# Performance work log

Measured on AMD Instinct MI355X. Metric: run time of the kernel, lower is better.

The kernel has to match this reference:

```python
import jax, jax.numpy as jnp
import numpy as np

IN_F = 1024
OUT_F = 1024
B, S = 8, 4096


def _pack_ternary(tern):
    # encoding: -1 -> 0, 0 -> 1, +1 -> 2; 4 values per byte, matching torch pack_ternary_weights
    enc = (tern + 1.0).astype(jnp.int32).reshape(-1)  # length divisible by 4 here
    return (enc[0::4] | (enc[1::4] << 2) | (enc[2::4] << 4) | (enc[3::4] << 6)).astype(jnp.int32)


def setup_inputs() -> dict:
    key = jax.random.key(0)
    kx, kw = jax.random.split(key)
    x = jax.random.normal(kx, (B, S, IN_F), dtype=jnp.float32)
    w = jax.random.normal(kw, (OUT_F, IN_F), dtype=jnp.float32) * 0.02
    # quantize_weights_158bit
    scale = jnp.maximum(jnp.mean(jnp.abs(w)), 1e-5)
    wn = w / scale
    tern = jnp.sign(wn) * (jnp.abs(wn) > 0.5).astype(jnp.float32)
    packed = _pack_ternary(tern)
    bias = jnp.zeros((OUT_F,), dtype=jnp.float32)
    return {"x": x, "packed_weight": packed, "weight_scale": scale.reshape(1), "bias": bias}


def reference(x, packed_weight, weight_scale, bias):
    n = OUT_F * IN_F
    shifts = jnp.array([0, 2, 4, 6], dtype=jnp.int32)
    # Faithful to original unpack_ternary_weights: concatenate bit-planes, then truncate.
    # (This is a permutation of the packed order, replicated deliberately.)
    enc = ((packed_weight[None, :] >> shifts[:, None]) & 3).reshape(-1)[:n]
    w = (enc.astype(jnp.float32) - 1.0).reshape(OUT_F, IN_F) * weight_scale  # dequant ternary
    # training path: INT8 per-token activation fake-quant
    act_scale = 127.0 / jnp.maximum(jnp.max(jnp.abs(x), axis=-1, keepdims=True), 1e-5)
    x_dq = jnp.clip(jnp.round(x * act_scale), -128.0, 127.0) / act_scale
    return jnp.einsum('bsi,oi->bso', x_dq, w) + bias
```

## Files before the change

kernel.cpp:

```cpp
#include <hip/hip_runtime.h>
#include <hip/hip_bf16.h>
#include <stdint.h>

typedef int i32x4 __attribute__((ext_vector_type(4)));

constexpr int IN_F = 1024;
constexpr int OUT_F = 1024;
constexpr int M_TOT = 8 * 4096;
constexpr int K_TOT = 1024;
constexpr int N_TOT = 1024;

__global__ __launch_bounds__(256) void quant_kernel(
    const float* __restrict__ x,
    const float* __restrict__ wscale,
    const int* __restrict__ packed,
    int8_t* __restrict__ q,
    float* __restrict__ inv_row,
    int8_t* __restrict__ wt)
{
    const int row = blockIdx.x;
    const int t = threadIdx.x;
    const float4 v = reinterpret_cast<const float4*>(x + (size_t)row * IN_F)[t];
    float m = fmaxf(fmaxf(fabsf(v.x), fabsf(v.y)), fmaxf(fabsf(v.z), fabsf(v.w)));
    #pragma unroll
    for (int off = 32; off > 0; off >>= 1)
        m = fmaxf(m, __shfl_xor(m, off));
    __shared__ float smax[4];
    if ((t & 63) == 0) smax[t >> 6] = m;
    __syncthreads();
    m = fmaxf(fmaxf(smax[0], smax[1]), fmaxf(smax[2], smax[3]));
    const float a = fmaxf(m, 1e-5f);
    const float as = 127.0f / a;

    char4 o;
    o.x = (char)(int)fminf(fmaxf(rintf(v.x * as), -128.0f), 127.0f);
    o.y = (char)(int)fminf(fmaxf(rintf(v.y * as), -128.0f), 127.0f);
    o.z = (char)(int)fminf(fmaxf(rintf(v.z * as), -128.0f), 127.0f);
    o.w = (char)(int)fminf(fmaxf(rintf(v.w * as), -128.0f), 127.0f);
    reinterpret_cast<char4*>(q + (size_t)row * IN_F)[t] = o;
    if (t == 0) inv_row[row] = (a / 127.0f) * wscale[0];

    if (row < OUT_F) {
        const int oo = row;
        const int k0 = t * 4;
        const int sh = (oo >> 8) * 2;
        const int pbase = ((oo & 255) << 10) + k0;
        const int4 pw = *reinterpret_cast<const int4*>(packed + pbase);
        char4 r;
        r.x = (char)(((pw.x >> sh) & 3) - 1);
        r.y = (char)(((pw.y >> sh) & 3) - 1);
        r.z = (char)(((pw.z >> sh) & 3) - 1);
        r.w = (char)(((pw.w >> sh) & 3) - 1);
        *reinterpret_cast<char4*>(wt + (size_t)oo * IN_F + k0) = r;
    }
}

constexpr int BM = 256, BN = 256, BK = 128;
constexpr int NT = K_TOT / BK;

__global__ __launch_bounds__(512, 2) void gemm_kernel(
    const int8_t* __restrict__ qa,
    const int8_t* __restrict__ wb,
    const float* __restrict__ inv_row,
    const float* __restrict__ bias,
    float* __restrict__ out)
{
    int bid = blockIdx.x;
    bid = (bid & 7) * ((int)gridDim.x >> 3) + (bid >> 3);
    const int tm = bid >> 2;
    const int tn = bid & 3;

    const int tid = threadIdx.x;
    const int lane = tid & 63;
    const int wid = tid >> 6;
    const int wr = wid >> 2;
    const int wc = wid & 3;

    __shared__ int8_t lds[2][2][2][128 * 128];

    const int rowA0 = tm * BM;
    const int rowB0 = tn * BN;
    const int frow = lane & 15;
    const int fq = lane >> 4;

    i32x4 acc[8][4] = {};

    auto stage = [&](int buf, int ab, int region, int kt) {
        const int8_t* base = ab ? wb : qa;
        #pragma unroll
        for (int j = 0; j < 2; ++j) {
            const int c = j * 512 + tid;
            const int rl = c >> 3, cc = c & 7;
            const int grow = ab ? (rowB0 + region * 128 + rl)
                                : (rowA0 + (rl & 64) * 2 + region * 64 + (rl & 63));
            const int scc = cc ^ (rl & 7);
            const int8_t* src = base + (size_t)grow * K_TOT + kt * BK + scc * 16;
            __builtin_amdgcn_global_load_lds(
                (const __attribute__((address_space(1))) void*)src,
                (__attribute__((address_space(3))) void*)&lds[buf][ab][region][c * 16],
                16, 0, 0);
        }
    };

    auto ldA = [&](int buf, int region, int mf, int ks) -> i32x4 {
        const int local = wr * 64 + (mf & 3) * 16 + frow;
        const int ch = (ks * 4 + fq) ^ (local & 7);
        return *reinterpret_cast<const i32x4*>(&lds[buf][0][region][local * 128 + ch * 16]);
    };
    auto ldB = [&](int buf, int nf, int ks) -> i32x4 {
        const int region = wc >> 1;
        const int local = (wc & 1) * 64 + nf * 16 + frow;
        const int ch = (ks * 4 + fq) ^ (local & 7);
        return *reinterpret_cast<const i32x4*>(&lds[buf][1][region][local * 128 + ch * 16]);
    };

    i32x4 aF[4][2], bF[4][2], aG[4][2];

    stage(0, 1, 0, 0); stage(0, 1, 1, 0); stage(0, 0, 0, 0); stage(0, 0, 1, 0);
    asm volatile("s_waitcnt vmcnt(0)" ::: "memory");
    __builtin_amdgcn_s_barrier();
    #pragma unroll
    for (int mf = 0; mf < 4; ++mf)
        #pragma unroll
        for (int ks = 0; ks < 2; ++ks)
            aF[mf][ks] = ldA(0, 0, mf, ks);
    #pragma unroll
    for (int nf = 0; nf < 4; ++nf)
        #pragma unroll
        for (int ks = 0; ks < 2; ++ks)
            bF[nf][ks] = ldB(0, nf, ks);

    #pragma unroll 1
    for (int T = 0; T < NT; ++T) {
        const int cur = T & 1, nxt = cur ^ 1;
        const bool st = (T + 1 < NT);

        #pragma unroll
        for (int mf = 0; mf < 4; ++mf)
            #pragma unroll
            for (int ks = 0; ks < 2; ++ks)
                aG[mf][ks] = ldA(cur, 1, mf, ks);
        if (st) {
            stage(nxt, 1, 0, T + 1); stage(nxt, 1, 1, T + 1);
            stage(nxt, 0, 0, T + 1); stage(nxt, 0, 1, T + 1);
        }

        asm volatile("s_waitcnt lgkmcnt(8)" ::: "memory");
        __builtin_amdgcn_sched_barrier(0);
        __builtin_amdgcn_s_setprio(1);
        #pragma unroll
        for (int mf = 0; mf < 4; ++mf)
            #pragma unroll
            for (int nf = 0; nf < 4; ++nf)
                #pragma unroll
                for (int ks = 0; ks < 2; ++ks)
                    acc[mf][nf] = __builtin_amdgcn_mfma_i32_16x16x64_i8(
                        aF[mf][ks], bF[nf][ks], acc[mf][nf], 0, 0, 0);
        __builtin_amdgcn_s_setprio(0);

        asm volatile("s_waitcnt lgkmcnt(0)" ::: "memory");
        __builtin_amdgcn_sched_barrier(0);
        __builtin_amdgcn_s_setprio(1);
        #pragma unroll
        for (int mf = 0; mf < 4; ++mf)
            #pragma unroll
            for (int nf = 0; nf < 4; ++nf)
                #pragma unroll
                for (int ks = 0; ks < 2; ++ks)
                    acc[4 + mf][nf] = __builtin_amdgcn_mfma_i32_16x16x64_i8(
                        aG[mf][ks], bF[nf][ks], acc[4 + mf][nf], 0, 0, 0);
        __builtin_amdgcn_s_setprio(0);

        if (st) {
            asm volatile("s_waitcnt vmcnt(0)" ::: "memory");
            __builtin_amdgcn_s_barrier();
            #pragma unroll
            for (int mf = 0; mf < 4; ++mf)
                #pragma unroll
                for (int ks = 0; ks < 2; ++ks)
                    aF[mf][ks] = ldA(nxt, 0, mf, ks);
            #pragma unroll
            for (int nf = 0; nf < 4; ++nf)
                #pragma unroll
                for (int ks = 0; ks < 2; ++ks)
                    bF[nf][ks] = ldB(nxt, nf, ks);
        }
    }

    #pragma unroll
    for (int mi = 0; mi < 8; ++mi) {
        #pragma unroll
        for (int j = 0; j < 4; ++j) {
            const int gm = rowA0 + wr * 128 + mi * 16 + fq * 4 + j;
            const float sc = inv_row[gm];
            #pragma unroll
            for (int nf = 0; nf < 4; ++nf) {
                const int gn = rowB0 + wc * 64 + nf * 16 + frow;
                __builtin_nontemporal_store(
                    (float)acc[mi][nf][j] * sc + bias[gn],
                    &out[(size_t)gm * N_TOT + gn]);
            }
        }
    }
}

extern "C" void kernel_launch(void* const* d_in, const int* in_sizes, int n_in,
                              void* d_out, int out_size, void* d_ws, size_t ws_size,
                              hipStream_t stream) {
    const float* x = (const float*)d_in[0];
    const int* packed = (const int*)d_in[1];
    const float* wscale = (const float*)d_in[2];
    const float* bias = (const float*)d_in[3];
    float* out = (float*)d_out;

    int8_t* q = (int8_t*)d_ws;
    int8_t* wt = (int8_t*)((char*)d_ws + (size_t)M_TOT * K_TOT);
    float* inv_row = (float*)((char*)d_ws + (size_t)M_TOT * K_TOT + (size_t)N_TOT * K_TOT);

    quant_kernel<<<M_TOT, 256, 0, stream>>>(x, wscale, packed, q, inv_row, wt);
    gemm_kernel<<<(M_TOT / BM) * (N_TOT / BN), 512, 0, stream>>>(q, wt, inv_row, bias, out);
}
```

Before: 86.24 us.

## Split B operand into LDS-staged half and direct-to-register global loads

The weight matrix is rewritten by the quant kernel into a k-tiled, swizzled layout so each 64-wide k slice is contiguous per output column. In the GEMM, half of each 128-wide B k-tile is staged through a smaller LDS buffer and the other half is loaded straight from global memory into registers a tile ahead. The aim is to cut LDS footprint and LDS read traffic for B, which could raise occupancy or relieve LDS bandwidth. In exchange it adds register pressure and exposes direct global-load latency inside the MFMA loop.

```diff
diff --git a/kernel.cpp b/kernel.cpp
--- a/kernel.cpp
+++ b/kernel.cpp
@@ -16,7 +16,7 @@
     const int* __restrict__ packed,
     int8_t* __restrict__ q,
     float* __restrict__ inv_row,
-    int8_t* __restrict__ wt)
+    int8_t* __restrict__ wt2)
 {
     const int row = blockIdx.x;
     const int t = threadIdx.x;
@@ -51,7 +51,11 @@
         r.y = (char)(((pw.y >> sh) & 3) - 1);
         r.z = (char)(((pw.z >> sh) & 3) - 1);
         r.w = (char)(((pw.w >> sh) & 3) - 1);
-        *reinterpret_cast<char4*>(wt + (size_t)oo * IN_F + k0) = r;
+        const int kt64 = k0 >> 6;
+        const int kq = (k0 >> 4) & 3;
+        const int kqs = kq ^ ((oo >> 1) & 3);
+        const int addr = kt64 * 65536 + oo * 64 + kqs * 16 + (k0 & 15);
+        *reinterpret_cast<char4*>(wt2 + addr) = r;
     }
 }
 
@@ -60,7 +64,7 @@
 
 __global__ __launch_bounds__(512, 2) void gemm_kernel(
     const int8_t* __restrict__ qa,
-    const int8_t* __restrict__ wb,
+    const int8_t* __restrict__ wt2,
     const float* __restrict__ inv_row,
     const float* __restrict__ bias,
     float* __restrict__ out)
@@ -76,7 +80,8 @@
     const int wr = wid >> 2;
     const int wc = wid & 3;
 
-    __shared__ int8_t lds[2][2][2][128 * 128];
+    __shared__ int8_t ldsA[2][2][128 * 128];
+    __shared__ int8_t ldsB[2][256 * 64];
 
     const int rowA0 = tm * BM;
     const int rowB0 = tn * BN;
@@ -85,19 +90,28 @@
 
     i32x4 acc[8][4] = {};
 
-    auto stage = [&](int buf, int ab, int region, int kt) {
-        const int8_t* base = ab ? wb : qa;
+    auto stageA = [&](int buf, int region, int kt) {
         #pragma unroll
         for (int j = 0; j < 2; ++j) {
             const int c = j * 512 + tid;
             const int rl = c >> 3, cc = c & 7;
-            const int grow = ab ? (rowB0 + region * 128 + rl)
-                                : (rowA0 + (rl & 64) * 2 + region * 64 + (rl & 63));
+            const int grow = rowA0 + (rl & 64) * 2 + region * 64 + (rl & 63);
             const int scc = cc ^ (rl & 7);
-            const int8_t* src = base + (size_t)grow * K_TOT + kt * BK + scc * 16;
+            const int8_t* src = qa + (size_t)grow * K_TOT + kt * BK + scc * 16;
             __builtin_amdgcn_global_load_lds(
                 (const __attribute__((address_space(1))) void*)src,
-                (__attribute__((address_space(3))) void*)&lds[buf][ab][region][c * 16],
+                (__attribute__((address_space(3))) void*)&ldsA[buf][region][c * 16],
+                16, 0, 0);
+        }
+    };
+    auto stageB = [&](int buf, int T) {
+        #pragma unroll
+        for (int j = 0; j < 2; ++j) {
+            const int c = j * 512 + tid;
+            const int8_t* src = wt2 + (size_t)(2 * T) * 65536 + (size_t)rowB0 * 64 + c * 16;
+            __builtin_amdgcn_global_load_lds(
+                (const __attribute__((address_space(1))) void*)src,
+                (__attribute__((address_space(3))) void*)&ldsB[buf][c * 16],
                 16, 0, 0);
         }
     };
@@ -105,18 +119,28 @@
     auto ldA = [&](int buf, int region, int mf, int ks) -> i32x4 {
         const int local = wr * 64 + (mf & 3) * 16 + frow;
         const int ch = (ks * 4 + fq) ^ (local & 7);
-        return *reinterpret_cast<const i32x4*>(&lds[buf][0][region][local * 128 + ch * 16]);
-    };
-    auto ldB = [&](int buf, int nf, int ks) -> i32x4 {
-        const int region = wc >> 1;
-        const int local = (wc & 1) * 64 + nf * 16 + frow;
-        const int ch = (ks * 4 + fq) ^ (local & 7);
-        return *reinterpret_cast<const i32x4*>(&lds[buf][1][region][local * 128 + ch * 16]);
-    };
-
-    i32x4 aF[4][2], bF[4][2], aG[4][2];
-
-    stage(0, 1, 0, 0); stage(0, 1, 1, 0); stage(0, 0, 0, 0); stage(0, 0, 1, 0);
+        return *reinterpret_cast<const i32x4*>(&ldsA[buf][region][local * 128 + ch * 16]);
+    };
+    auto ldBL = [&](int buf, int nf) -> i32x4 {
+        const int col = wc * 64 + nf * 16 + frow;
+        const int kqs = fq ^ ((col >> 1) & 3);
+        return *reinterpret_cast<const i32x4*>(&ldsB[buf][col * 64 + kqs * 16]);
+    };
+
+    const int gc0 = wc * 64 + frow;
+    const int8_t* wbD = wt2 + (size_t)(rowB0 + gc0) * 64 + (fq ^ ((gc0 >> 1) & 3)) * 16;
+
+    i32x4 aF[4][2], aG[4][2], bFL[4], bD0[4], bD1[4];
+
+    auto loadBD = [&](int T, i32x4 (&b)[4]) {
+        #pragma unroll
+        for (int nf = 0; nf < 4; ++nf)
+            b[nf] = *reinterpret_cast<const i32x4*>(
+                wbD + (size_t)(2 * T + 1) * 65536 + nf * 1024);
+    };
+
+    stageA(0, 0, 0); stageA(0, 1, 0); stageB(0, 0);
+    loadBD(0, bD0);
     asm volatile("s_waitcnt vmcnt(0)" ::: "memory");
     __builtin_amdgcn_s_barrier();
     #pragma unroll
@@ -126,24 +150,20 @@
             aF[mf][ks] = ldA(0, 0, mf, ks);
     #pragma unroll
     for (int nf = 0; nf < 4; ++nf)
-        #pragma unroll
-        for (int ks = 0; ks < 2; ++ks)
-            bF[nf][ks] = ldB(0, nf, ks);
-
-    #pragma unroll 1
-    for (int T = 0; T < NT; ++T) {
+        bFL[nf] = ldBL(0, nf);
+
+    auto body = [&](int T, i32x4 (&bDcur)[4], i32x4 (&bDnxt)[4]) {
         const int cur = T & 1, nxt = cur ^ 1;
         const bool st = (T + 1 < NT);
 
+        if (st) loadBD(T + 1, bDnxt);
+
         #pragma unroll
         for (int mf = 0; mf < 4; ++mf)
             #pragma unroll
             for (int ks = 0; ks < 2; ++ks)
                 aG[mf][ks] = ldA(cur, 1, mf, ks);
-        if (st) {
-            stage(nxt, 1, 0, T + 1); stage(nxt, 1, 1, T + 1);
-            stage(nxt, 0, 0, T + 1); stage(nxt, 0, 1, T + 1);
-        }
+        if (st) { stageA(nxt, 0, T + 1); stageA(nxt, 1, T + 1); stageB(nxt, T + 1); }
 
         asm volatile("s_waitcnt lgkmcnt(8)" ::: "memory");
         __builtin_amdgcn_sched_barrier(0);
@@ -151,11 +171,12 @@
         #pragma unroll
         for (int mf = 0; mf < 4; ++mf)
             #pragma unroll
-            for (int nf = 0; nf < 4; ++nf)
-                #pragma unroll
-                for (int ks = 0; ks < 2; ++ks)
-                    acc[mf][nf] = __builtin_amdgcn_mfma_i32_16x16x64_i8(
-                        aF[mf][ks], bF[nf][ks], acc[mf][nf], 0, 0, 0);
+            for (int nf = 0; nf < 4; ++nf) {
+                acc[mf][nf] = __builtin_amdgcn_mfma_i32_16x16x64_i8(
+                    aF[mf][0], bFL[nf], acc[mf][nf], 0, 0, 0);
+                acc[mf][nf] = __builtin_amdgcn_mfma_i32_16x16x64_i8(
+                    aF[mf][1], bDcur[nf], acc[mf][nf], 0, 0, 0);
+            }
         __builtin_amdgcn_s_setprio(0);
 
         asm volatile("s_waitcnt lgkmcnt(0)" ::: "memory");
@@ -164,11 +185,12 @@
         #pragma unroll
         for (int mf = 0; mf < 4; ++mf)
             #pragma unroll
-            for (int nf = 0; nf < 4; ++nf)
-                #pragma unroll
-                for (int ks = 0; ks < 2; ++ks)
-                    acc[4 + mf][nf] = __builtin_amdgcn_mfma_i32_16x16x64_i8(
-                        aG[mf][ks], bF[nf][ks], acc[4 + mf][nf], 0, 0, 0);
+            for (int nf = 0; nf < 4; ++nf) {
+                acc[4 + mf][nf] = __builtin_amdgcn_mfma_i32_16x16x64_i8(
+                    aG[mf][0], bFL[nf], acc[4 + mf][nf], 0, 0, 0);
+                acc[4 + mf][nf] = __builtin_amdgcn_mfma_i32_16x16x64_i8(
+                    aG[mf][1], bDcur[nf], acc[4 + mf][nf], 0, 0, 0);
+            }
         __builtin_amdgcn_s_setprio(0);
 
         if (st) {
@@ -181,10 +203,14 @@
                     aF[mf][ks] = ldA(nxt, 0, mf, ks);
             #pragma unroll
             for (int nf = 0; nf < 4; ++nf)
-                #pragma unroll
-                for (int ks = 0; ks < 2; ++ks)
-                    bF[nf][ks] = ldB(nxt, nf, ks);
-        }
+                bFL[nf] = ldBL(nxt, nf);
+        }
+    };
+
+    #pragma unroll 1
+    for (int t2 = 0; t2 < NT; t2 += 2) {
+        body(t2, bD0, bD1);
+        body(t2 + 1, bD1, bD0);
     }
 
     #pragma unroll
@@ -214,9 +240,9 @@
     float* out = (float*)d_out;
 
     int8_t* q = (int8_t*)d_ws;
-    int8_t* wt = (int8_t*)((char*)d_ws + (size_t)M_TOT * K_TOT);
+    int8_t* wt2 = (int8_t*)((char*)d_ws + (size_t)M_TOT * K_TOT);
     float* inv_row = (float*)((char*)d_ws + (size_t)M_TOT * K_TOT + (size_t)N_TOT * K_TOT);
 
-    quant_kernel<<<M_TOT, 256, 0, stream>>>(x, wscale, packed, q, inv_row, wt);
-    gemm_kernel<<<(M_TOT / BM) * (N_TOT / BN), 512, 0, stream>>>(q, wt, inv_row, bias, out);
+    quant_kernel<<<M_TOT, 256, 0, stream>>>(x, wscale, packed, q, inv_row, wt2);
+    gemm_kernel<<<(M_TOT / BM) * (N_TOT / BN), 512, 0, stream>>>(q, wt2, inv_row, bias, out);
 }
```

Result: slower. 105.5 us (+22.3%).
